# Optimization experiments

Hardware: AMD Instinct MI355X
Metric: run time of the kernel (lower is better)

## Reference

```python
import jax, jax.numpy as jnp
import numpy as np

H = 32          # query heads
KVH = 8         # kv heads (GQA)
D = 128         # head dim
GROUP = 128     # quantization group size along K
THETA = 10000.0 # RoPE base


def dequant_fp4(codes, scales):
    """FP4 E2M1-style dequant: w = (code - 8) * 0.5 * per-group scale.
    codes: [K, N] int32 in [0,16); scales: [K//GROUP, N] float32."""
    K, N = codes.shape
    g = K // GROUP
    w = (codes.astype(jnp.float32) - 8.0) * 0.5
    return (w.reshape(g, GROUP, N) * scales[:, None, :]).reshape(K, N)


def apply_rope(x, pos):
    """x: [B, S, h, D]; rotate-half RoPE."""
    half = D // 2
    inv_freq = 1.0 / (THETA ** (jnp.arange(half, dtype=jnp.float32) / half))
    ang = pos.astype(jnp.float32)[:, None] * inv_freq[None, :]  # [S, half]
    cos = jnp.cos(ang)[None, :, None, :]
    sin = jnp.sin(ang)[None, :, None, :]
    x1, x2 = x[..., :half], x[..., half:]
    return jnp.concatenate([x1 * cos - x2 * sin, x2 * cos + x1 * sin], axis=-1)


def setup_inputs() -> dict:
    key = jax.random.key(0)
    ks = jax.random.split(key, 9)
    B, S, HID = 1, 2048, H * D
    KV = KVH * D
    x = jax.random.normal(ks[0], (B, S, HID), dtype=jnp.float32)
    q_codes = jax.random.randint(ks[1], (HID, HID), 0, 16, dtype=jnp.int32)
    k_codes = jax.random.randint(ks[2], (HID, KV), 0, 16, dtype=jnp.int32)
    v_codes = jax.random.randint(ks[3], (HID, KV), 0, 16, dtype=jnp.int32)
    o_codes = jax.random.randint(ks[4], (HID, HID), 0, 16, dtype=jnp.int32)
    g = HID // GROUP
    mk = lambda k, n: jax.random.uniform(k, (g, n), dtype=jnp.float32) * 0.02 + 1e-3
    q_scales = mk(ks[5], HID)
    k_scales = mk(ks[6], KV)
    v_scales = mk(ks[7], KV)
    o_scales = mk(ks[8], HID)
    return {"x": x, "q_codes": q_codes, "k_codes": k_codes, "v_codes": v_codes,
            "o_codes": o_codes, "q_scales": q_scales, "k_scales": k_scales,
            "v_scales": v_scales, "o_scales": o_scales}


def reference(x, q_codes, k_codes, v_codes, o_codes,
              q_scales, k_scales, v_scales, o_scales):
    B, S, _ = x.shape
    Wq = dequant_fp4(q_codes, q_scales)  # [HID, HID]
    Wk = dequant_fp4(k_codes, k_scales)  # [HID, KVH*D]
    Wv = dequant_fp4(v_codes, v_scales)
    Wo = dequant_fp4(o_codes, o_scales)

    q = (x @ Wq).reshape(B, S, H, D)
    k = (x @ Wk).reshape(B, S, KVH, D)
    v = (x @ Wv).reshape(B, S, KVH, D)

    pos = jnp.arange(S)
    q = apply_rope(q, pos)
    k = apply_rope(k, pos)

    # GQA: expand kv heads to query heads (this is what reading the shared
    # KV cache per query-head group computes)
    rep = H // KVH
    k = jnp.repeat(k, rep, axis=2)  # [B, S, H, D]
    v = jnp.repeat(v, rep, axis=2)

    scale = 1.0 / jnp.sqrt(jnp.float32(D))
    scores = jnp.einsum('bqhd,bkhd->bhqk', q, k) * scale  # [B, H, S, S]
    causal = jnp.tril(jnp.ones((S, S), dtype=bool))
    scores = jnp.where(causal[None, None], scores, jnp.float32(-1e30))
    probs = jax.nn.softmax(scores, axis=-1)
    attn = jnp.einsum('bhqk,bkhd->bqhd', probs, v).reshape(B, S, H * D)
    return attn @ Wo
```

## Files before the change

kernel.cpp:

```cpp
#include <hip/hip_runtime.h>

typedef unsigned short u16;
typedef __attribute__((ext_vector_type(4))) float f32x4;
typedef __attribute__((ext_vector_type(4))) unsigned short u16x4;
typedef __attribute__((ext_vector_type(8))) short bf16x8;

#define S_LEN 2048
#define NH 32
#define NKVH 8
#define DHEAD 128
#define HID 4096
#define KVW 1024
#define QKVW 6144

__device__ __forceinline__ u16 f2bf(float f) {
  unsigned u = __float_as_uint(f);
  u = u + 0x7fffu + ((u >> 16) & 1u);
  return (u16)(u >> 16);
}
__device__ __forceinline__ float bf2f(u16 h) {
  return __uint_as_float(((unsigned)h) << 16);
}
__device__ __forceinline__ void async16(void* lds, const void* g) {
  __builtin_amdgcn_global_load_lds((const __attribute__((address_space(1))) void*)g,
                                   (__attribute__((address_space(3))) void*)lds, 16, 0, 0);
}
__device__ __forceinline__ f32x4 mfma16(bf16x8 a, bf16x8 b, f32x4 c) {
  return __builtin_amdgcn_mfma_f32_16x16x32_bf16(a, b, c, 0, 0, 0);
}
__device__ __forceinline__ unsigned cvtpk(float a, float b) {
  unsigned r;
  asm("v_cvt_pk_bf16_f32 %0, %1, %2" : "=v"(r) : "v"(a), "v"(b));
  return r;
}

__global__ __launch_bounds__(256) void f2bf4_kernel(const float* __restrict__ in,
                                                    u16* __restrict__ out) {
  size_t i = ((size_t)blockIdx.x * 256 + threadIdx.x) * 4;
  f32x4 v = *(const f32x4*)(in + i);
  u16x4 o;
  o.x = f2bf(v.x); o.y = f2bf(v.y); o.z = f2bf(v.z); o.w = f2bf(v.w);
  *(u16x4*)(out + i) = o;
}

__global__ __launch_bounds__(256) void dequant_t_kernel(const int* __restrict__ codes,
                                                        const float* __restrict__ scales,
                                                        u16* __restrict__ Wt,
                                                        int K, int N) {
  __shared__ float tile[32][33];
  const int tx = threadIdx.x & 31, ty = threadIdx.x >> 5;
  const int k0 = blockIdx.x * 32, n0 = blockIdx.y * 32;
  const float sc = scales[(size_t)(k0 >> 7) * N + n0 + tx];
#pragma unroll
  for (int i = 0; i < 4; ++i) {
    int k = k0 + ty + i * 8;
    int c = codes[(size_t)k * N + n0 + tx];
    tile[ty + i * 8][tx] = ((float)c - 8.0f) * 0.5f * sc;
  }
  __syncthreads();
#pragma unroll
  for (int i = 0; i < 4; ++i) {
    int n = n0 + ty + i * 8;
    Wt[(size_t)n * K + k0 + tx] = f2bf(tile[tx][ty + i * 8]);
  }
}

template <int NI, int OUTF32>
__global__ __launch_bounds__(512, 2) void gemm_w(const u16* __restrict__ A, int lda,
                                                 const u16* __restrict__ Bt, int ldb,
                                                 void* __restrict__ Cv, int ldc, int K) {
  constexpr int BN = NI * 32;
  constexpr int NB = NI / 2;
  constexpr int BSLOT = BN * 128;
  extern __shared__ char lds[];
  char* Bbase = lds + 65536;
  const int tid = threadIdx.x, w = tid >> 6, lane = tid & 63;
  const int lo = lane & 15, hi = lane >> 4;
  const int wm = w >> 1, wn = w & 1;
  const int id = blockIdx.x;
  const int g = id & 7, r = id >> 3;
  const int bm = r >> 2, bn = g * 4 + (r & 3);
  const int m0 = bm * 256, n0 = bn * BN;

  const int srow = tid >> 3, schunk = (tid & 7) ^ (srow & 7);
  const char* Ab = (const char*)(A + (size_t)(m0 + srow) * lda) + schunk * 16;
  const char* Bb = (const char*)(Bt + (size_t)(n0 + srow) * ldb) + schunk * 16;

  f32x4 acc[4][NI];
#pragma unroll
  for (int i = 0; i < 4; ++i)
#pragma unroll
    for (int j = 0; j < NI; ++j) acc[i][j] = (f32x4){0.f, 0.f, 0.f, 0.f};

  auto stageA = [&](int buf, int k1) {
#pragma unroll
    for (int u = 0; u < 2; ++u) {
      char* dst = lds + buf * 32768 + u * 8192 + w * 1024;
      async16(dst, Ab + ((size_t)(u * 64) * lda + k1) * 2);
      async16(dst + 16384, Ab + ((size_t)(u * 64 + 128) * lda + k1) * 2);
    }
  };
  auto stageB = [&](int slot, int k1) {
#pragma unroll
    for (int j = 0; j < NB; ++j)
      async16(Bbase + slot * BSLOT + j * 8192 + w * 1024,
              Bb + ((size_t)(j * 64) * ldb + k1) * 2);
  };

  const int xm = (lo & 7) << 4;
  const int aro = (wm >> 1) * 16384 + (wm & 1) * 8192 + lo * 128;
  int bofs[NI];
#pragma unroll
  for (int ni = 0; ni < NI; ++ni) {
    int n = wn * (NI * 16) + ni * 16 + lo;
    bofs[ni] = (n >> 6) * 8192 + (n & 63) * 128;
  }

  auto ldfrags = [&](const char* As, const char* Bs, int kk, bf16x8* Afo, bf16x8* Bfo) {
    const int ck = (kk * 64 + hi * 16) ^ xm;
#pragma unroll
    for (int i = 0; i < 4; ++i) Afo[i] = *(const bf16x8*)(As + aro + i * 2048 + ck);
#pragma unroll
    for (int ni = 0; ni < NI; ++ni) Bfo[ni] = *(const bf16x8*)(Bs + bofs[ni] + ck);
  };

  stageA(0, 0);
  stageB(0, 0);
  stageB(1, 64);
  asm volatile("s_waitcnt vmcnt(%0)" ::"i"(NB) : "memory");
  __builtin_amdgcn_s_barrier();

  bf16x8 Afc[4], Bfc[NI], Afn[4], Bfn[NI];
  ldfrags(lds, Bbase, 0, Afc, Bfc);

  const int KT = K >> 6;
  int ab = 0, bb = 0;
  for (int t = 0; t < KT; ++t) {
    const char* As = lds + ab * 32768;
    const char* Bs = Bbase + bb * BSLOT;
    const bool m1 = t + 1 < KT, m2 = t + 2 < KT;
    int bs2 = bb + 2; if (bs2 >= 3) bs2 -= 3;
    int bn1 = bb + 1; if (bn1 >= 3) bn1 -= 3;
    if (m1) stageA(ab ^ 1, (t + 1) << 6);
    ldfrags(As, Bs, 1, Afn, Bfn);
    __builtin_amdgcn_sched_barrier(0);
    __builtin_amdgcn_s_setprio(1);
#pragma unroll
    for (int i = 0; i < 4; ++i)
#pragma unroll
      for (int ni = 0; ni < NI; ++ni)
        acc[i][ni] = mfma16(Afc[i], Bfc[ni], acc[i][ni]);
    __builtin_amdgcn_s_setprio(0);
    if (m2) stageB(bs2, (t + 2) << 6);
    __builtin_amdgcn_s_setprio(1);
#pragma unroll
    for (int i = 0; i < 4; ++i)
#pragma unroll
      for (int ni = 0; ni < NI; ++ni)
        acc[i][ni] = mfma16(Afn[i], Bfn[ni], acc[i][ni]);
    __builtin_amdgcn_s_setprio(0);
    if (m1) {
      if (m2) asm volatile("s_waitcnt vmcnt(%0)" ::"i"(NB) : "memory");
      else    asm volatile("s_waitcnt vmcnt(0)" ::: "memory");
      __builtin_amdgcn_s_barrier();
      ldfrags(lds + (ab ^ 1) * 32768, Bbase + bn1 * BSLOT, 0, Afc, Bfc);
      __builtin_amdgcn_sched_barrier(0);
    }
    ab ^= 1;
    if (++bb == 3) bb = 0;
  }
#pragma unroll
  for (int mi = 0; mi < 4; ++mi)
#pragma unroll
    for (int ni = 0; ni < NI; ++ni) {
      size_t row = (size_t)(m0 + wm * 64 + mi * 16 + hi * 4);
      size_t col = (size_t)(n0 + wn * (NI * 16) + ni * 16 + lo);
#pragma unroll
      for (int rr = 0; rr < 4; ++rr) {
        size_t idx = (row + rr) * ldc + col;
        if (OUTF32) ((float*)Cv)[idx] = acc[mi][ni][rr];
        else ((u16*)Cv)[idx] = f2bf(acc[mi][ni][rr]);
      }
    }
}

__global__ void rope_tab_kernel(float* __restrict__ ctab, float* __restrict__ stab) {
  int s = blockIdx.x, d = threadIdx.x;
  float inv = exp2f(-(float)d * 0.2076205059304601f);
  float ang = (float)s * inv;
  ctab[s * 64 + d] = cosf(ang);
  stab[s * 64 + d] = sinf(ang);
}

__global__ __launch_bounds__(256) void rope_kernel(u16* __restrict__ qkv,
                                                   const float* __restrict__ ctab,
                                                   const float* __restrict__ stab) {
  int s = blockIdx.x;
  int head = blockIdx.y * 4 + (threadIdx.x >> 6);
  int d = threadIdx.x & 63;
  int col = head < NH ? head * DHEAD + d : HID + (head - NH) * DHEAD + d;
  size_t base = (size_t)s * QKVW + col;
  float c = ctab[s * 64 + d], sn = stab[s * 64 + d];
  float x1 = bf2f(qkv[base]);
  float x2 = bf2f(qkv[base + 64]);
  qkv[base] = f2bf(x1 * c - x2 * sn);
  qkv[base + 64] = f2bf(x2 * c + x1 * sn);
}

__global__ __launch_bounds__(256) void vtrans_kernel(const u16* __restrict__ qkv,
                                                     u16* __restrict__ Vt) {
  __shared__ u16 tile[32][33];
  const int tx = threadIdx.x & 31, ty = threadIdx.x >> 5;
  const int s0 = blockIdx.x * 32, c0 = blockIdx.y * 32;
#pragma unroll
  for (int i = 0; i < 4; ++i)
    tile[ty + i * 8][tx] = qkv[(size_t)(s0 + ty + i * 8) * QKVW + (HID + KVW) + c0 + tx];
  __syncthreads();
#pragma unroll
  for (int i = 0; i < 4; ++i)
    Vt[(size_t)(c0 + ty + i * 8) * S_LEN + s0 + tx] = tile[tx][ty + i * 8];
}

__global__ __launch_bounds__(256) void attn_kernel(const u16* __restrict__ qkv,
                                                   const u16* __restrict__ Vt,
                                                   u16* __restrict__ attnO) {
  __shared__ alignas(16) u16 Ks[2][64 * 128];
  __shared__ alignas(16) u16 Vs[2][128 * 64];
  __shared__ alignas(16) unsigned Ps32[4][16][44];
  const int tid = threadIdx.x, w = tid >> 6, lane = tid & 63;
  const int lo = lane & 15, hi = lane >> 4;
  const int bx = blockIdx.x, h = blockIdx.y, kvh = h >> 2;
  const u16* Kbase = qkv + HID + kvh * DHEAD;
  const u16* Vbase = Vt + (size_t)kvh * DHEAD * S_LEN;
  const int krow = w * 4 + hi;
  const int kscn = lo;
  const int vrow = w * 8 + (lane >> 3);
  const int vscn = lane & 7;

#pragma unroll 1
  for (int pass = 0; pass < 2; ++pass) {
    const int qb = pass == 0 ? (31 - bx) : bx;
    const int qrow0 = qb * 64 + w * 16;
    bf16x8 qf[4];
    {
      const u16* qp = qkv + (size_t)(qrow0 + lo) * QKVW + h * DHEAD;
      const float qs = 0.08838834764831845f * 1.4426950408889634f;
#pragma unroll
      for (int dc = 0; dc < 4; ++dc) {
        bf16x8 v = *(const bf16x8*)(qp + dc * 32 + hi * 8);
#pragma unroll
        for (int j = 0; j < 8; ++j) v[j] = (short)f2bf(bf2f((u16)v[j]) * qs);
        qf[dc] = v;
      }
    }
    f32x4 oacc[8];
#pragma unroll
    for (int i = 0; i < 8; ++i) oacc[i] = (f32x4){0.f, 0.f, 0.f, 0.f};
    float m_run = -1e30f, l_run = 0.f;

    const int nt = qb + 1;
#pragma unroll
    for (int i = 0; i < 4; ++i) {
      int kr = i * 16 + krow;
      async16((char*)&Ks[0][0] + (i * 16 + w * 4) * 256,
              (const char*)(Kbase + (size_t)kr * QKVW + (kscn ^ (kr & 7)) * 8));
      int vr = i * 32 + vrow;
      async16((char*)&Vs[0][0] + (i * 32 + w * 8) * 128,
              (const char*)(Vbase + (size_t)vr * S_LEN + (vscn ^ (vr & 7)) * 8));
    }
    __syncthreads();
    for (int kt = 0; kt < nt; ++kt) {
      const int cur = kt & 1;
      if (kt + 1 < nt) {
#pragma unroll
        for (int i = 0; i < 4; ++i) {
          int kr = i * 16 + krow;
          async16((char*)&Ks[cur ^ 1][0] + (i * 16 + w * 4) * 256,
                  (const char*)(Kbase + (size_t)((kt + 1) * 64 + kr) * QKVW + (kscn ^ (kr & 7)) * 8));
          int vr = i * 32 + vrow;
          async16((char*)&Vs[cur ^ 1][0] + (i * 32 + w * 8) * 128,
                  (const char*)(Vbase + (size_t)vr * S_LEN + (kt + 1) * 64 + (vscn ^ (vr & 7)) * 8));
        }
      }
      f32x4 st[4];
#pragma unroll
      for (int t = 0; t < 4; ++t) st[t] = (f32x4){0.f, 0.f, 0.f, 0.f};
#pragma unroll
      for (int t = 0; t < 4; ++t) {
        int kq = t * 16 + lo;
#pragma unroll
        for (int dc = 0; dc < 4; ++dc) {
          bf16x8 kf = *(const bf16x8*)((const char*)&Ks[cur][0] + kq * 256 +
                                       (((dc << 2) + hi) ^ (kq & 7)) * 16);
          st[t] = mfma16(kf, qf[dc], st[t]);
        }
      }
      if (kt == qb) {
#pragma unroll
        for (int t = 0; t < 4; ++t)
#pragma unroll
          for (int r = 0; r < 4; ++r) {
            int kposl = t * 16 + 4 * hi + r;
            st[t][r] = (kposl <= w * 16 + lo) ? st[t][r] : -1e30f;
          }
      }
      float mloc = st[0][0];
#pragma unroll
      for (int t = 0; t < 4; ++t)
#pragma unroll
        for (int r = 0; r < 4; ++r) mloc = fmaxf(mloc, st[t][r]);
      mloc = fmaxf(mloc, __shfl_xor(mloc, 16, 64));
      mloc = fmaxf(mloc, __shfl_xor(mloc, 32, 64));
      if (!__all(mloc - m_run <= 8.0f)) {
        float mn = fmaxf(m_run, mloc);
        float alpha = exp2f(m_run - mn);
        m_run = mn;
        l_run *= alpha;
#pragma unroll
        for (int dt = 0; dt < 8; ++dt)
#pragma unroll
          for (int r = 0; r < 4; ++r) oacc[dt][r] *= alpha;
      }
      float psum = 0.f;
#pragma unroll
      for (int t = 0; t < 4; ++t)
#pragma unroll
        for (int r = 0; r < 4; ++r) {
          float p = exp2f(st[t][r] - m_run);
          st[t][r] = p;
          psum += p;
        }
      psum += __shfl_xor(psum, 16, 64);
      psum += __shfl_xor(psum, 32, 64);
      l_run += psum;
#pragma unroll
      for (int t = 0; t < 4; ++t)
#pragma unroll
        for (int rp = 0; rp < 2; ++rp)
          Ps32[w][lo][8 * t + 2 * hi + rp] = cvtpk(st[t][2 * rp], st[t][2 * rp + 1]);
      bf16x8 pf[2];
#pragma unroll
      for (int kc = 0; kc < 2; ++kc) pf[kc] = *(const bf16x8*)&Ps32[w][lo][kc * 16 + hi * 4];
#pragma unroll
      for (int dt = 0; dt < 8; ++dt) {
        int d = dt * 16 + lo;
#pragma unroll
        for (int kc = 0; kc < 2; ++kc) {
          bf16x8 vf = *(const bf16x8*)((const char*)&Vs[cur][0] + d * 128 +
                                       (((kc << 2) + hi) ^ (d & 7)) * 16);
          oacc[dt] = mfma16(vf, pf[kc], oacc[dt]);
        }
      }
      __syncthreads();
    }
    float linv = 1.0f / l_run;
    u16* op = attnO + (size_t)(qrow0 + lo) * HID + h * DHEAD;
#pragma unroll
    for (int dt = 0; dt < 8; ++dt) {
      u16x4 o4;
#pragma unroll
      for (int r = 0; r < 4; ++r) o4[r] = f2bf(oacc[dt][r] * linv);
      *(u16x4*)(op + dt * 16 + 4 * hi) = o4;
    }
  }
}

extern "C" void kernel_launch(void* const* d_in, const int* in_sizes, int n_in,
                              void* d_out, int out_size, void* d_ws, size_t ws_size,
                              hipStream_t stream) {
  const float* x = (const float*)d_in[0];
  const int* qc = (const int*)d_in[1];
  const int* kc = (const int*)d_in[2];
  const int* vc = (const int*)d_in[3];
  const int* oc = (const int*)d_in[4];
  const float* qs = (const float*)d_in[5];
  const float* ks = (const float*)d_in[6];
  const float* vs = (const float*)d_in[7];
  const float* os = (const float*)d_in[8];
  float* out = (float*)d_out;
  char* ws = (char*)d_ws;

  u16* xb    = (u16*)(ws);
  u16* qkv   = (u16*)(ws + 16777216);
  u16* attnb = (u16*)(ws + 41943040);
  u16* Vt    = (u16*)(ws + 58720256);
  u16* Wbig  = (u16*)(ws + 62914560);
  float* ctab = (float*)Vt;
  float* stab = (float*)(ws + 58720256 + 524288);

  f2bf4_kernel<<<8192, 256, 0, stream>>>(x, xb);
  dequant_t_kernel<<<dim3(128, 128), 256, 0, stream>>>(qc, qs, Wbig, HID, HID);
  dequant_t_kernel<<<dim3(128, 32), 256, 0, stream>>>(kc, ks, Wbig + (size_t)HID * HID, HID, KVW);
  dequant_t_kernel<<<dim3(128, 32), 256, 0, stream>>>(vc, vs, Wbig + (size_t)(HID + KVW) * HID, HID, KVW);
  rope_tab_kernel<<<2048, 64, 0, stream>>>(ctab, stab);
  gemm_w<6, 0><<<256, 512, 139264, stream>>>(xb, HID, Wbig, HID, qkv, QKVW, HID);
  rope_kernel<<<dim3(S_LEN, (NH + NKVH) / 4), 256, 0, stream>>>(qkv, ctab, stab);
  vtrans_kernel<<<dim3(64, 32), 256, 0, stream>>>(qkv, Vt);
  attn_kernel<<<dim3(16, 32), 256, 0, stream>>>(qkv, Vt, attnb);
  dequant_t_kernel<<<dim3(128, 128), 256, 0, stream>>>(oc, os, Wbig, HID, HID);
  gemm_w<4, 1><<<256, 512, 114688, stream>>>(attnb, HID, Wbig, HID, out, HID, HID);
}
```

Before: 322.7 us.

## Single-buffer attention K/V tiles to raise occupancy and swizzle P scratch

Removes the double-buffered K/V shared-memory staging in the attention kernel and loads each tile synchronously at the start of every iteration, which halves LDS use. It raises launch bounds to 4 blocks per CU to exploit the freed LDS. It also shrinks the P scratch rows to 32 words and applies an XOR swizzle to avoid bank conflicts. In exchange, the prefetch overlap of the next tile with compute is lost, so each iteration now waits on global loads, and any latency hiding has to come from more resident waves.

```diff
diff --git a/kernel.cpp b/kernel.cpp
--- a/kernel.cpp
+++ b/kernel.cpp
@@ -221,14 +221,15 @@
     Vt[(size_t)(c0 + ty + i * 8) * S_LEN + s0 + tx] = tile[tx][ty + i * 8];
 }
 
-__global__ __launch_bounds__(256) void attn_kernel(const u16* __restrict__ qkv,
-                                                   const u16* __restrict__ Vt,
-                                                   u16* __restrict__ attnO) {
-  __shared__ alignas(16) u16 Ks[2][64 * 128];
-  __shared__ alignas(16) u16 Vs[2][128 * 64];
-  __shared__ alignas(16) unsigned Ps32[4][16][44];
+__global__ __launch_bounds__(256, 4) void attn_kernel(const u16* __restrict__ qkv,
+                                                      const u16* __restrict__ Vt,
+                                                      u16* __restrict__ attnO) {
+  __shared__ alignas(16) u16 Ks[64 * 128];
+  __shared__ alignas(16) u16 Vs[128 * 64];
+  __shared__ alignas(16) unsigned Ps32[4][16][32];
   const int tid = threadIdx.x, w = tid >> 6, lane = tid & 63;
   const int lo = lane & 15, hi = lane >> 4;
+  const unsigned pxor = (unsigned)((lo & 7) << 2);
   const int bx = blockIdx.x, h = blockIdx.y, kvh = h >> 2;
   const u16* Kbase = qkv + HID + kvh * DHEAD;
   const u16* Vbase = Vt + (size_t)kvh * DHEAD * S_LEN;
@@ -259,29 +260,17 @@
     float m_run = -1e30f, l_run = 0.f;
 
     const int nt = qb + 1;
-#pragma unroll
-    for (int i = 0; i < 4; ++i) {
-      int kr = i * 16 + krow;
-      async16((char*)&Ks[0][0] + (i * 16 + w * 4) * 256,
-              (const char*)(Kbase + (size_t)kr * QKVW + (kscn ^ (kr & 7)) * 8));
-      int vr = i * 32 + vrow;
-      async16((char*)&Vs[0][0] + (i * 32 + w * 8) * 128,
-              (const char*)(Vbase + (size_t)vr * S_LEN + (vscn ^ (vr & 7)) * 8));
-    }
-    __syncthreads();
     for (int kt = 0; kt < nt; ++kt) {
-      const int cur = kt & 1;
-      if (kt + 1 < nt) {
-#pragma unroll
-        for (int i = 0; i < 4; ++i) {
-          int kr = i * 16 + krow;
-          async16((char*)&Ks[cur ^ 1][0] + (i * 16 + w * 4) * 256,
-                  (const char*)(Kbase + (size_t)((kt + 1) * 64 + kr) * QKVW + (kscn ^ (kr & 7)) * 8));
-          int vr = i * 32 + vrow;
-          async16((char*)&Vs[cur ^ 1][0] + (i * 32 + w * 8) * 128,
-                  (const char*)(Vbase + (size_t)vr * S_LEN + (kt + 1) * 64 + (vscn ^ (vr & 7)) * 8));
-        }
-      }
+#pragma unroll
+      for (int i = 0; i < 4; ++i) {
+        int kr = i * 16 + krow;
+        async16((char*)&Ks[0] + (i * 16 + w * 4) * 256,
+                (const char*)(Kbase + (size_t)(kt * 64 + kr) * QKVW + (kscn ^ (kr & 7)) * 8));
+        int vr = i * 32 + vrow;
+        async16((char*)&Vs[0] + (i * 32 + w * 8) * 128,
+                (const char*)(Vbase + (size_t)vr * S_LEN + kt * 64 + (vscn ^ (vr & 7)) * 8));
+      }
+      __syncthreads();
       f32x4 st[4];
 #pragma unroll
       for (int t = 0; t < 4; ++t) st[t] = (f32x4){0.f, 0.f, 0.f, 0.f};
@@ -290,7 +279,7 @@
         int kq = t * 16 + lo;
 #pragma unroll
         for (int dc = 0; dc < 4; ++dc) {
-          bf16x8 kf = *(const bf16x8*)((const char*)&Ks[cur][0] + kq * 256 +
+          bf16x8 kf = *(const bf16x8*)((const char*)&Ks[0] + kq * 256 +
                                        (((dc << 2) + hi) ^ (kq & 7)) * 16);
           st[t] = mfma16(kf, qf[dc], st[t]);
         }
@@ -337,16 +326,18 @@
       for (int t = 0; t < 4; ++t)
 #pragma unroll
         for (int rp = 0; rp < 2; ++rp)
-          Ps32[w][lo][8 * t + 2 * hi + rp] = cvtpk(st[t][2 * rp], st[t][2 * rp + 1]);
+          Ps32[w][lo][(unsigned)(8 * t + 2 * hi + rp) ^ pxor] =
+              cvtpk(st[t][2 * rp], st[t][2 * rp + 1]);
       bf16x8 pf[2];
 #pragma unroll
-      for (int kc = 0; kc < 2; ++kc) pf[kc] = *(const bf16x8*)&Ps32[w][lo][kc * 16 + hi * 4];
+      for (int kc = 0; kc < 2; ++kc)
+        pf[kc] = *(const bf16x8*)&Ps32[w][lo][(unsigned)(kc * 16 + hi * 4) ^ pxor];
 #pragma unroll
       for (int dt = 0; dt < 8; ++dt) {
         int d = dt * 16 + lo;
 #pragma unroll
         for (int kc = 0; kc < 2; ++kc) {
-          bf16x8 vf = *(const bf16x8*)((const char*)&Vs[cur][0] + d * 128 +
+          bf16x8 vf = *(const bf16x8*)((const char*)&Vs[0] + d * 128 +
                                        (((kc << 2) + hi) ^ (d & 7)) * 16);
           oacc[dt] = mfma16(vf, pf[kc], oacc[dt]);
         }
```

New measurement: 318.2 us (median of 3 runs). Within noise of the previous version (-1.4%).
